# Kernel optimization log

Measured on AMD Instinct MI355X. Metric: run time of the kernel, lower is better.

Reference implementation:

```python
import jax, jax.numpy as jnp
import numpy as np

BLOCK_DIMS = [(512, 512), (512, 512), (512, 512)]
OUTPUT_SIZE = 10
BATCH = 65536
BN_EPS = 1e-5


def sign_ste(x):
    # Binarize = sign() with straight-through estimator (torch code mutates .data,
    # so autograd sees identity). Forward value is exactly jnp.sign(x).
    return x + jax.lax.stop_gradient(jnp.sign(x) - x)


def setup_inputs() -> dict:
    key = jax.random.key(0)
    ks = jax.random.split(key, 2 + 6 * len(BLOCK_DIMS) + 2)
    it = iter(ks)
    x = jax.random.normal(next(it), (BATCH, BLOCK_DIMS[0][0]), dtype=jnp.float32)
    Ws, bs, gammas, betas = [], [], [], []
    for (din, dout) in BLOCK_DIMS:
        lim = 1.0 / np.sqrt(din)
        Ws.append(jax.random.uniform(next(it), (dout, din), jnp.float32, -lim, lim))
        bs.append(jax.random.uniform(next(it), (dout,), jnp.float32, -lim, lim))
        gammas.append(jnp.ones((dout,), jnp.float32))
        betas.append(jnp.zeros((dout,), jnp.float32))
        next(it); next(it)  # burn keys for determinism symmetry
    din = BLOCK_DIMS[-1][1]
    lim = 1.0 / np.sqrt(din)
    W_out = jax.random.uniform(next(it), (OUTPUT_SIZE, din), jnp.float32, -lim, lim)
    b_out = jax.random.uniform(next(it), (OUTPUT_SIZE,), jnp.float32, -lim, lim)
    return {"x": x, "Ws": Ws, "bs": bs, "gammas": gammas, "betas": betas,
            "W_out": W_out, "b_out": b_out}


def reference(x, Ws, bs, gammas, betas, W_out, b_out):
    # x.view(-1, input_size) then Binarize(x); BinarizeLinear re-binarizes its
    # input (sign is idempotent) and binarizes its weight, keeps float bias.
    h = sign_ste(x)
    for W, b, g, be in zip(Ws, bs, gammas, betas):
        h = jnp.einsum('bi,oi->bo', sign_ste(h), sign_ste(W)) + b
        # BatchNorm1d in training mode: biased batch statistics over the batch dim
        mu = jnp.mean(h, axis=0)
        var = jnp.var(h, axis=0)
        h = (h - mu) * jax.lax.rsqrt(var + BN_EPS) * g + be
        h = jnp.clip(h, -1.0, 1.0)  # Hardtanh
    h = jnp.einsum('bi,oi->bo', sign_ste(h), sign_ste(W_out)) + b_out
    return jax.nn.log_softmax(h, axis=-1)
```

## Files before the change

kernel.cpp:

```cpp
#include <hip/hip_runtime.h>
#include <stdint.h>

typedef unsigned long long u64;
typedef unsigned int u32;

#define BATCH   65536
#define DIN     512
#define NW      8
#define NCLS    10
#define RPB     64
#define NSL     16


__device__ u64 g_bits[2][BATCH * NW];
__device__ u64 g_mask[2][BATCH * NW];
__device__ u64 g_rowflag[2][BATCH / 64];
__device__ int g_cp0[NSL * DIN + 4];
__device__ int g_cp1[NSL * DIN];
__device__ int g_S1[DIN];
__device__ int g_fastflag[4];
__device__ u64 g_wbitsT3[3][NW * DIN];
__device__ u64 g_wmaskT3[3][NW * DIN];
__device__ u64 g_obits[NCLS * NW];
__device__ u64 g_omask[NCLS * NW];

__device__ __forceinline__ int* cpbase(int sel) { return sel ? g_cp1 : g_cp0; }
#define WZ_OFF (NSL * DIN)

__global__ __launch_bounds__(512) void k_zero()
{
    const int t = blockIdx.x * 512 + threadIdx.x;
    for (int k = t; k < NSL * DIN + 4; k += 16 * 512)
        g_cp0[k] = 0;
}

__global__ __launch_bounds__(256) void k_prep_all(
    const float* __restrict__ x,
    const float* __restrict__ W0, const float* __restrict__ W1,
    const float* __restrict__ W2,
    const float* __restrict__ g0, const float* __restrict__ b0,
    const float* __restrict__ g1, const float* __restrict__ b1,
    const float* __restrict__ g2, const float* __restrict__ b2,
    const float* __restrict__ Wout)
{
    __shared__ int csB[DIN];
    __shared__ u64 AZ[4];
    const int tid = threadIdx.x, lane = tid & 63, wv = tid >> 6;
    const int b = blockIdx.x;
    const int gwave = b * 4 + wv;

    if (gwave < 3 * DIN) {
        const int layer = gwave >> 9, row = gwave & (DIN - 1);
        const float* W = (layer == 0) ? W0 : (layer == 1) ? W1 : W2;
        const float4* p = (const float4*)(W + (size_t)row * DIN + lane * 8);
        float4 v0 = p[0], v1 = p[1];
        float f[8] = {v0.x, v0.y, v0.z, v0.w, v1.x, v1.y, v1.z, v1.w};
        u32 byteS = 0, byteM = 0;
#pragma unroll
        for (int j = 0; j < 8; j++) {
            u32 pos = f[j] > 0.0f;
            u32 nz  = f[j] != 0.0f;
            byteS |= pos << j;
            byteM |= nz << j;
        }
        u64 wS = 0, wM = 0;
        const int src = (lane & 7) * 8;
#pragma unroll
        for (int j = 0; j < 8; j++) {
            wS |= (u64)(__shfl((int)byteS, src + j) & 0xFF) << (8 * j);
            wM |= (u64)(__shfl((int)byteM, src + j) & 0xFF) << (8 * j);
        }
        if (lane < 8) {
            g_wbitsT3[layer][(size_t)lane * DIN + row] = wS;
            g_wmaskT3[layer][(size_t)lane * DIN + row] = wM;
        }
        u64 ok = __ballot(byteM == 0xFFu);
        if (lane == 0 && ok != ~0ull) atomicOr(&g_cp0[WZ_OFF + layer], 1);
    } else if (gwave < 3 * DIN + NCLS) {
        const int row = gwave - 3 * DIN;
        const float4* p = (const float4*)(Wout + (size_t)row * DIN + lane * 8);
        float4 v0 = p[0], v1 = p[1];
        float f[8] = {v0.x, v0.y, v0.z, v0.w, v1.x, v1.y, v1.z, v1.w};
        u32 byteS = 0, byteM = 0;
#pragma unroll
        for (int j = 0; j < 8; j++) {
            u32 pos = f[j] > 0.0f;
            u32 nz  = f[j] != 0.0f;
            byteS |= pos << j;
            byteM |= nz << j;
        }
        u64 wS = 0, wM = 0;
        const int src = (lane & 7) * 8;
#pragma unroll
        for (int j = 0; j < 8; j++) {
            wS |= (u64)(__shfl((int)byteS, src + j) & 0xFF) << (8 * j);
            wM |= (u64)(__shfl((int)byteM, src + j) & 0xFF) << (8 * j);
        }
        if (lane < 8) {
            g_obits[row * NW + lane] = wS;
            g_omask[row * NW + lane] = wM;
        }
    } else if (gwave < 3 * DIN + NCLS + 3) {
        const int layer = gwave - (3 * DIN + NCLS);
        const float* gp = (layer == 0) ? g0 : (layer == 1) ? g1 : g2;
        const float* bp = (layer == 0) ? b0 : (layer == 1) ? b1 : b2;
        bool allok = true;
#pragma unroll
        for (int j = 0; j < 8; j++) {
            float gv = gp[j * 64 + lane], bv = bp[j * 64 + lane];
            allok &= (__ballot((gv > 0.0f) && (bv == 0.0f)) == ~0ull);
        }
        if (lane == 0) g_fastflag[layer] = allok ? 1 : 0;
    }

    for (int i = tid; i < DIN; i += 256) csB[i] = 0;
    __syncthreads();
    int cs[8];
#pragma unroll
    for (int j = 0; j < 8; j++) cs[j] = 0;
    u64 zb = 0;
    const int rbase = b * 64 + wv * 16;

    auto proc = [&](int row, int rb, float4 v0, float4 v1) {
        float f[8] = {v0.x, v0.y, v0.z, v0.w, v1.x, v1.y, v1.z, v1.w};
        u32 byteS = 0, byteM = 0;
#pragma unroll
        for (int j = 0; j < 8; j++) {
            u32 pos = f[j] > 0.0f;
            u32 nz  = f[j] != 0.0f;
            byteS |= pos << j;
            byteM |= nz << j;
            cs[j] += nz ? (pos ? 1 : -1) : 0;
        }
        u64 wS = 0, wM = 0;
        const int src = (lane & 7) * 8;
#pragma unroll
        for (int j = 0; j < 8; j++) {
            wS |= (u64)(__shfl((int)byteS, src + j) & 0xFF) << (8 * j);
            wM |= (u64)(__shfl((int)byteM, src + j) & 0xFF) << (8 * j);
        }
        u64 ok = __ballot(byteM == 0xFFu);
        if (lane < 8)
            g_bits[0][(size_t)row * NW + lane] = wS;
        if (ok != ~0ull) {
            if (lane < 8) g_mask[0][(size_t)row * NW + lane] = wM;
            zb |= 1ull << rb;
        }
    };

    for (int k = 0; k < 16; k += 2) {
        const int rowA = rbase + k, rowB = rowA + 1;
        const float4* pA = (const float4*)(x + (size_t)rowA * DIN + lane * 8);
        const float4* pB = (const float4*)(x + (size_t)rowB * DIN + lane * 8);
        float4 a0 = pA[0], a1 = pA[1];
        float4 c0 = pB[0], c1 = pB[1];
        proc(rowA, wv * 16 + k,     a0, a1);
        proc(rowB, wv * 16 + k + 1, c0, c1);
    }
#pragma unroll
    for (int j = 0; j < 8; j++)
        if (cs[j]) atomicAdd(&csB[lane * 8 + j], cs[j]);
    if (lane == 0) AZ[wv] = zb;
    __syncthreads();
    if (tid == 0) g_rowflag[0][b] = AZ[0] | AZ[1] | AZ[2] | AZ[3];
    for (int i = tid; i < DIN; i += 256) {
        int v = csB[i];
        if (v) atomicAdd(&g_cp0[(b & (NSL - 1)) * DIN + i], v);
    }
}

__global__ __launch_bounds__(512) void k_s1(int sel, int layer)
{
    const int so = sel ^ 1;
    __shared__ int csL[DIN];
    const int tid = threadIdx.x;
    const int t1 = blockIdx.x * 512 + tid;
    {
        int* cpn = cpbase(so);
        if (t1 < NSL * DIN) cpn[t1] = 0;
        if (t1 < BATCH / 64) g_rowflag[so][t1] = 0;
    }
    {
        const int* cps = cpbase(sel);
        int s = 0;
#pragma unroll
        for (int p = 0; p < NSL; p++) s += cps[p * DIN + tid];
        csL[tid] = s;
    }
    __syncthreads();
    const int lane = tid & 63, wv = tid >> 6;
    const int row = blockIdx.x * 8 + wv;
    u64 wS_h = 0, wM_h = 0;
    if (lane < 8) {
        wS_h = g_wbitsT3[layer][(size_t)lane * DIN + row];
        wM_h = g_wmaskT3[layer][(size_t)lane * DIN + row];
    }
    const u64 wS = __shfl(wS_h, lane >> 3);
    const u64 wM = __shfl(wM_h, lane >> 3);
    const u32 s8 = (u32)(wS >> (8 * (lane & 7))) & 0xFF;
    const u32 m8 = (u32)(wM >> (8 * (lane & 7))) & 0xFF;
    int acc = 0;
#pragma unroll
    for (int k = 0; k < 8; k++) {
        int c = csL[lane * 8 + k];
        int v = ((s8 >> k) & 1) ? c : -c;
        acc += ((m8 >> k) & 1) ? v : 0;
    }
#pragma unroll
    for (int o = 32; o; o >>= 1) acc += __shfl_down(acc, o);
    if (lane == 0) g_S1[row] = acc;
}

template<int FINAL>
__global__ __launch_bounds__(256, 4) void k_bingemm(int sel, int layer,
        const float* __restrict__ gamma, const float* __restrict__ beta,
        const float* __restrict__ bout, float* __restrict__ out)
{
    const int so = sel ^ 1;
    __shared__ alignas(16) u64 AT[RPB * NW];
    __shared__ u64 AZ[FINAL ? 1 : 4];
    __shared__ u64 SB[FINAL ? RPB * 9 : 1];
    __shared__ u64 SM[FINAL ? RPB * 9 : 1];
    __shared__ float ZR[FINAL ? RPB * 11 : 1];
    const int tid  = threadIdx.x;
    const int lane = tid & 63;
    const int wv   = tid >> 6;
    const int rowBase = blockIdx.x * RPB;
    const u64* wbT = g_wbitsT3[layer];
    const u64* wmT = g_wmaskT3[layer];
    int* cpo = cpbase(so);

    {
        ulonglong2* dst = (ulonglong2*)AT;
        const ulonglong2* src = (const ulonglong2*)&g_bits[sel][(size_t)rowBase * NW];
        dst[tid] = src[tid];
    }
    const int col0 = wv * 128 + lane;
    const int col1 = col0 + 64;
    u64 w0[8], w1[8];
#pragma unroll
    for (int c = 0; c < 8; c++) {
        w0[c] = wbT[c * DIN + col0];
        w1[c] = wbT[c * DIN + col1];
    }
    const int thr0 = g_S1[col0];
    const int thr1 = g_S1[col1];
    const int R0 = (DIN << 16) - thr0, R1 = (DIN << 16) - thr1;
    const int tg0 = (R0 + ((1 << 17) - 1)) >> 17, tl0 = (R0 >> 17) + 1;
    const int tg1 = (R1 + ((1 << 17) - 1)) >> 17, tl1 = (R1 >> 17) + 1;
    const u64 rflags = g_rowflag[sel][blockIdx.x];
    const bool slowAll = (g_fastflag[layer] == 0) || (g_cp0[WZ_OFF + layer] != 0);
    const bool noTie = __all((tg0 == tl0) && (tg1 == tl1));
    int cs0 = 0, cs1 = 0;
    u64 mB0 = 0, mB1 = 0, mM0 = 0, mM1 = 0;
    u64 anyz = 0;
    __syncthreads();

    if (!slowAll && rflags == 0 && noTie) {
        mM0 = ~0ull; mM1 = ~0ull;
        int n0 = 0, n1 = 0;
#pragma unroll 4
        for (int r = 0; r < RPB; r++) {
            const ulonglong2* Av = (const ulonglong2*)(AT + r * NW);
            ulonglong2 A0 = Av[0], A1 = Av[1], A2 = Av[2], A3 = Av[3];
            const u64 aw[8] = {A0.x, A0.y, A1.x, A1.y, A2.x, A2.y, A3.x, A3.y};
            int P0 = 0, P1 = 0;
#pragma unroll
            for (int c = 0; c < 8; c++) {
                P0 += __popcll(aw[c] ^ w0[c]);
                P1 += __popcll(aw[c] ^ w1[c]);
            }
            bool gb0 = P0 < tg0, gb1 = P1 < tg1;
            u64 gt0 = __ballot(gb0);
            u64 gt1 = __ballot(gb1);
            n0 += (int)gb0; n1 += (int)gb1;
            bool mine = (lane == r);
            mB0 = mine ? gt0 : mB0;  mB1 = mine ? gt1 : mB1;
        }
        cs0 = 2 * n0 - RPB;
        cs1 = 2 * n1 - RPB;
    } else if (!slowAll && rflags == 0) {
#pragma unroll 4
        for (int r = 0; r < RPB; r++) {
            const ulonglong2* Av = (const ulonglong2*)(AT + r * NW);
            ulonglong2 A0 = Av[0], A1 = Av[1], A2 = Av[2], A3 = Av[3];
            const u64 aw[8] = {A0.x, A0.y, A1.x, A1.y, A2.x, A2.y, A3.x, A3.y};
            int P0 = 0, P1 = 0;
#pragma unroll
            for (int c = 0; c < 8; c++) {
                P0 += __popcll(aw[c] ^ w0[c]);
                P1 += __popcll(aw[c] ^ w1[c]);
            }
            bool gb0 = P0 < tg0, lb0 = P0 >= tl0;
            bool gb1 = P1 < tg1, lb1 = P1 >= tl1;
            u64 gt0 = __ballot(gb0), nz0 = gt0 | __ballot(lb0);
            u64 gt1 = __ballot(gb1), nz1 = gt1 | __ballot(lb1);
            cs0 += (int)gb0 - (int)lb0;
            cs1 += (int)gb1 - (int)lb1;
            bool mine = (lane == r);
            mB0 = mine ? gt0 : mB0;  mB1 = mine ? gt1 : mB1;
            mM0 = mine ? nz0 : mM0;  mM1 = mine ? nz1 : mM1;
            if ((nz0 & nz1) != ~0ull) {
                anyz |= 1ull << r;
                if (lane == 0)
                    atomicOr(&g_rowflag[so][(rowBase + r) >> 6],
                             1ull << ((rowBase + r) & 63));
            }
        }
    } else {
        double td0 = 0.0, td1 = 0.0;
        int md0 = 0, md1 = 0;
        {
            float g = gamma[col0], be = beta[col0];
            int S1v = thr0;
            td0 = (double)S1v;
            if (g != 0.0f) {
                md0 = (g > 0.0f) ? 0 : 1;
                if (be != 0.0f) {
                    double s = rsqrt((double)DIN + 1e-5);
                    td0 = (double)S1v - 65536.0 * (double)be / (s * (double)g);
                }
            } else md0 = (be > 0.0f) ? 2 : ((be < 0.0f) ? 3 : 4);
            g = gamma[col1]; be = beta[col1]; S1v = thr1;
            td1 = (double)S1v;
            if (g != 0.0f) {
                md1 = (g > 0.0f) ? 0 : 1;
                if (be != 0.0f) {
                    double s = rsqrt((double)DIN + 1e-5);
                    td1 = (double)S1v - 65536.0 * (double)be / (s * (double)g);
                }
            } else md1 = (be > 0.0f) ? 2 : ((be < 0.0f) ? 3 : 4);
        }
        for (int r = 0; r < RPB; r++) {
            const bool fl = (rflags >> r) & 1;
            int bit0, bit1;
            if (!slowAll && !fl) {
                int P0 = 0, P1 = 0;
#pragma unroll
                for (int c = 0; c < 8; c++) {
                    u64 a = AT[r * NW + c];
                    P0 += __popcll(a ^ w0[c]);
                    P1 += __popcll(a ^ w1[c]);
                }
                int v0 = (DIN - 2 * P0) << 16;
                int v1 = (DIN - 2 * P1) << 16;
                bit0 = (v0 > thr0) - (v0 < thr0);
                bit1 = (v1 > thr1) - (v1 < thr1);
            } else {
                const int row = rowBase + r;
                int P0 = 0, Q0 = 0, P1 = 0, Q1 = 0;
#pragma unroll
                for (int c = 0; c < 8; c++) {
                    u64 a  = AT[r * NW + c];
                    u64 am = fl ? g_mask[sel][(size_t)row * NW + c] : ~0ull;
                    u64 m0 = am & wmT[c * DIN + col0];
                    u64 m1 = am & wmT[c * DIN + col1];
                    P0 += __popcll((a ^ w0[c]) & m0);  Q0 += __popcll(m0);
                    P1 += __popcll((a ^ w1[c]) & m1);  Q1 += __popcll(m1);
                }
                double Ds0 = (double)(Q0 - 2 * P0) * 65536.0;
                double Ds1 = (double)(Q1 - 2 * P1) * 65536.0;
                int c0 = (Ds0 > td0) ? 1 : ((Ds0 < td0) ? -1 : 0);
                int c1 = (Ds1 > td1) ? 1 : ((Ds1 < td1) ? -1 : 0);
                bit0 = (md0 == 0) ? c0 : (md0 == 1) ? -c0
                     : (md0 == 2) ? 1 : (md0 == 3) ? -1 : 0;
                bit1 = (md1 == 0) ? c1 : (md1 == 1) ? -c1
                     : (md1 == 2) ? 1 : (md1 == 3) ? -1 : 0;
            }
            u64 gt0 = __ballot(bit0 > 0), nz0 = __ballot(bit0 != 0);
            u64 gt1 = __ballot(bit1 > 0), nz1 = __ballot(bit1 != 0);
            cs0 += bit0;
            cs1 += bit1;
            bool mine = (lane == r);
            mB0 = mine ? gt0 : mB0;  mB1 = mine ? gt1 : mB1;
            mM0 = mine ? nz0 : mM0;  mM1 = mine ? nz1 : mM1;
            if ((nz0 & nz1) != ~0ull) {
                anyz |= 1ull << r;
                if (lane == 0)
                    atomicOr(&g_rowflag[so][(rowBase + r) >> 6],
                             1ull << ((rowBase + r) & 63));
            }
        }
    }

    if constexpr (FINAL) {
        SB[lane * 9 + 2 * wv]     = mB0;
        SB[lane * 9 + 2 * wv + 1] = mB1;
        SM[lane * 9 + 2 * wv]     = mM0;
        SM[lane * 9 + 2 * wv + 1] = mM1;
        __syncthreads();
        u64 b[NW], m[NW];
#pragma unroll
        for (int c = 0; c < NW; c++) { b[c] = SB[lane * 9 + c]; m[c] = SM[lane * 9 + c]; }
        const int cls0 = (wv < 2) ? wv * 3 : 2 + wv * 2;
        const int ncl  = (wv < 2) ? 3 : 2;
        for (int k = 0; k < ncl; k++) {
            const int o = cls0 + k;
            int P = 0, P2 = 0;
#pragma unroll
            for (int c = 0; c < NW; c++) {
                u64 om = g_omask[o * NW + c];
                u64 mm = m[c] & om;
                P  += __popcll((b[c] ^ g_obits[o * NW + c]) & mm);
                P2 += __popcll(mm);
            }
            ZR[lane * 11 + o] = (float)(P2 - 2 * P) + bout[o];
        }
        __syncthreads();
        if (wv == 0) {
            float z[NCLS], mx = -1e30f;
#pragma unroll
            for (int o = 0; o < NCLS; o++) { z[o] = ZR[lane * 11 + o]; mx = fmaxf(mx, z[o]); }
            float s = 0.0f;
#pragma unroll
            for (int o = 0; o < NCLS; o++) s += expf(z[o] - mx);
            float l = logf(s);
            float2* o2 = (float2*)(out + (size_t)(rowBase + lane) * NCLS);
#pragma unroll
            for (int p = 0; p < 5; p++) {
                float2 v;
                v.x = z[2 * p]     - mx - l;
                v.y = z[2 * p + 1] - mx - l;
                o2[p] = v;
            }
        }
    } else {
        AZ[wv] = anyz;
        __syncthreads();
        const u64 rowz = AZ[0] | AZ[1] | AZ[2] | AZ[3];
        size_t bofs = (size_t)(rowBase + lane) * NW + 2 * wv;
        ulonglong2 vb; vb.x = mB0; vb.y = mB1;
        *(ulonglong2*)&g_bits[so][bofs] = vb;
        if ((rowz >> lane) & 1) {
            ulonglong2 vm; vm.x = mM0; vm.y = mM1;
            *(ulonglong2*)&g_mask[so][bofs] = vm;
        }
        atomicAdd(&cpo[(blockIdx.x & (NSL - 1)) * DIN + col0], cs0);
        atomicAdd(&cpo[(blockIdx.x & (NSL - 1)) * DIN + col1], cs1);
    }
}

extern "C" void kernel_launch(void* const* d_in, const int* in_sizes, int n_in,
                              void* d_out, int out_size, void* d_ws, size_t ws_size,
                              hipStream_t stream)
{
    const float *x = 0, *Wl[3] = {0,0,0}, *gl[3] = {0,0,0}, *bl[3] = {0,0,0};
    const float *Wout = 0, *bout = 0;
    {
        int i = 0;
        x = (const float*)d_in[i++];
        if (i < n_in && in_sizes[i] == 3 * DIN * DIN) {
            for (int l = 0; l < 3; l++) Wl[l] = (const float*)d_in[i] + (size_t)l * DIN * DIN;
            i++;
        } else {
            for (int l = 0; l < 3 && i < n_in; l++) Wl[l] = (const float*)d_in[i++];
        }
        if (i < n_in && in_sizes[i] == 3 * DIN) i++;
        else i += 3;
        if (i < n_in && in_sizes[i] == 3 * DIN) {
            for (int l = 0; l < 3; l++) gl[l] = (const float*)d_in[i] + (size_t)l * DIN;
            i++;
        } else {
            for (int l = 0; l < 3 && i < n_in; l++) gl[l] = (const float*)d_in[i++];
        }
        if (i < n_in && in_sizes[i] == 3 * DIN) {
            for (int l = 0; l < 3; l++) bl[l] = (const float*)d_in[i] + (size_t)l * DIN;
            i++;
        } else {
            for (int l = 0; l < 3 && i < n_in; l++) bl[l] = (const float*)d_in[i++];
        }
        if (i < n_in) Wout = (const float*)d_in[i++];
        if (i < n_in) bout = (const float*)d_in[i++];
    }
    float* out = (float*)d_out;
    (void)out_size; (void)d_ws; (void)ws_size;

    k_zero<<<16, 512, 0, stream>>>();
    k_prep_all<<<1024, 256, 0, stream>>>(x, Wl[0], Wl[1], Wl[2],
                                         gl[0], bl[0], gl[1], bl[1], gl[2], bl[2],
                                         Wout);
    k_s1<<<64, 512, 0, stream>>>(0, 0);
    k_bingemm<0><<<BATCH / RPB, 256, 0, stream>>>(0, 0, gl[0], bl[0], bout, out);
    k_s1<<<64, 512, 0, stream>>>(1, 1);
    k_bingemm<0><<<BATCH / RPB, 256, 0, stream>>>(1, 1, gl[1], bl[1], bout, out);
    k_s1<<<64, 512, 0, stream>>>(0, 2);
    k_bingemm<1><<<BATCH / RPB, 256, 0, stream>>>(0, 2, gl[2], bl[2], bout, out);
}
```

Before: 338.9 us.

## Fold column-sum reduction into last-finishing block of preceding kernels

Removes the separate zeroing kernel and the three small k_s1 launches. The last block to finish each of prep and the first two GEMM layers, found through an atomic counter, now does the column-sum reduction and threshold computation. Zeroing of the counters and partial sums moves to the tail of the final GEMM, so the next call starts from clean state. The x-loading loop also issues four rows of loads per iteration instead of two. This cuts launch gaps, but one block now runs a serial tail of 512 rows on 256 threads, and correctness relies on the state left by the previous invocation.

```diff
diff --git a/kernel.cpp b/kernel.cpp
--- a/kernel.cpp
+++ b/kernel.cpp
@@ -15,8 +15,9 @@
 __device__ u64 g_bits[2][BATCH * NW];
 __device__ u64 g_mask[2][BATCH * NW];
 __device__ u64 g_rowflag[2][BATCH / 64];
-__device__ int g_cp0[NSL * DIN + 4];
+__device__ int g_cp0[NSL * DIN + 16];
 __device__ int g_cp1[NSL * DIN];
+__device__ int g_wzstash;
 __device__ int g_S1[DIN];
 __device__ int g_fastflag[4];
 __device__ u64 g_wbitsT3[3][NW * DIN];
@@ -25,13 +26,48 @@
 __device__ u64 g_omask[NCLS * NW];
 
 __device__ __forceinline__ int* cpbase(int sel) { return sel ? g_cp1 : g_cp0; }
-#define WZ_OFF (NSL * DIN)
-
-__global__ __launch_bounds__(512) void k_zero()
+#define WZ_OFF   (NSL * DIN)
+#define CNT_PREP (WZ_OFF + 4)
+#define CNT_G0   (WZ_OFF + 5)
+#define CNT_G1   (WZ_OFF + 6)
+#define CP0_TOT  (NSL * DIN + 16)
+
+__device__ void s1_tail(const int* __restrict__ cps, int layer,
+                        int* __restrict__ cpn, u64* __restrict__ rfn)
 {
-    const int t = blockIdx.x * 512 + threadIdx.x;
-    for (int k = t; k < NSL * DIN + 4; k += 16 * 512)
-        g_cp0[k] = 0;
+    __shared__ int csL[DIN];
+    const int tid = threadIdx.x;
+    for (int k = tid; k < NSL * DIN; k += 256) cpn[k] = 0;
+    for (int k = tid; k < BATCH / 64; k += 256) rfn[k] = 0;
+    for (int i = tid; i < DIN; i += 256) {
+        int s = 0;
+#pragma unroll
+        for (int p = 0; p < NSL; p++) s += cps[p * DIN + i];
+        csL[i] = s;
+    }
+    __syncthreads();
+    const int lane = tid & 63, wv = tid >> 6;
+    for (int row = wv; row < DIN; row += 4) {
+        u64 wS_h = 0, wM_h = 0;
+        if (lane < 8) {
+            wS_h = g_wbitsT3[layer][(size_t)lane * DIN + row];
+            wM_h = g_wmaskT3[layer][(size_t)lane * DIN + row];
+        }
+        const u64 wS = __shfl(wS_h, lane >> 3);
+        const u64 wM = __shfl(wM_h, lane >> 3);
+        const u32 s8 = (u32)(wS >> (8 * (lane & 7))) & 0xFF;
+        const u32 m8 = (u32)(wM >> (8 * (lane & 7))) & 0xFF;
+        int acc = 0;
+#pragma unroll
+        for (int k = 0; k < 8; k++) {
+            int c = csL[lane * 8 + k];
+            int v = ((s8 >> k) & 1) ? c : -c;
+            acc += ((m8 >> k) & 1) ? v : 0;
+        }
+#pragma unroll
+        for (int o = 32; o; o >>= 1) acc += __shfl_down(acc, o);
+        if (lane == 0) g_S1[row] = acc;
+    }
 }
 
 __global__ __launch_bounds__(256) void k_prep_all(
@@ -45,6 +81,7 @@
 {
     __shared__ int csB[DIN];
     __shared__ u64 AZ[4];
+    __shared__ int s_last;
     const int tid = threadIdx.x, lane = tid & 63, wv = tid >> 6;
     const int b = blockIdx.x;
     const int gwave = b * 4 + wv;
@@ -148,14 +185,20 @@
         }
     };
 
-    for (int k = 0; k < 16; k += 2) {
-        const int rowA = rbase + k, rowB = rowA + 1;
-        const float4* pA = (const float4*)(x + (size_t)rowA * DIN + lane * 8);
-        const float4* pB = (const float4*)(x + (size_t)rowB * DIN + lane * 8);
-        float4 a0 = pA[0], a1 = pA[1];
-        float4 c0 = pB[0], c1 = pB[1];
-        proc(rowA, wv * 16 + k,     a0, a1);
-        proc(rowB, wv * 16 + k + 1, c0, c1);
+    for (int k = 0; k < 16; k += 4) {
+        const int r0 = rbase + k;
+        const float4* p0 = (const float4*)(x + (size_t)r0 * DIN + lane * 8);
+        const float4* p1 = (const float4*)(x + (size_t)(r0 + 1) * DIN + lane * 8);
+        const float4* p2 = (const float4*)(x + (size_t)(r0 + 2) * DIN + lane * 8);
+        const float4* p3 = (const float4*)(x + (size_t)(r0 + 3) * DIN + lane * 8);
+        float4 a0 = p0[0], a1 = p0[1];
+        float4 b0v = p1[0], b1v = p1[1];
+        float4 c0 = p2[0], c1 = p2[1];
+        float4 d0 = p3[0], d1 = p3[1];
+        proc(r0,     wv * 16 + k,     a0, a1);
+        proc(r0 + 1, wv * 16 + k + 1, b0v, b1v);
+        proc(r0 + 2, wv * 16 + k + 2, c0, c1);
+        proc(r0 + 3, wv * 16 + k + 3, d0, d1);
     }
 #pragma unroll
     for (int j = 0; j < 8; j++)
@@ -167,48 +210,15 @@
         int v = csB[i];
         if (v) atomicAdd(&g_cp0[(b & (NSL - 1)) * DIN + i], v);
     }
-}
-
-__global__ __launch_bounds__(512) void k_s1(int sel, int layer)
-{
-    const int so = sel ^ 1;
-    __shared__ int csL[DIN];
-    const int tid = threadIdx.x;
-    const int t1 = blockIdx.x * 512 + tid;
-    {
-        int* cpn = cpbase(so);
-        if (t1 < NSL * DIN) cpn[t1] = 0;
-        if (t1 < BATCH / 64) g_rowflag[so][t1] = 0;
-    }
-    {
-        const int* cps = cpbase(sel);
-        int s = 0;
-#pragma unroll
-        for (int p = 0; p < NSL; p++) s += cps[p * DIN + tid];
-        csL[tid] = s;
-    }
+
+    __threadfence();
+    if (tid == 0)
+        s_last = (atomicAdd(&g_cp0[CNT_PREP], 1) == (int)gridDim.x - 1) ? 1 : 0;
     __syncthreads();
-    const int lane = tid & 63, wv = tid >> 6;
-    const int row = blockIdx.x * 8 + wv;
-    u64 wS_h = 0, wM_h = 0;
-    if (lane < 8) {
-        wS_h = g_wbitsT3[layer][(size_t)lane * DIN + row];
-        wM_h = g_wmaskT3[layer][(size_t)lane * DIN + row];
-    }
-    const u64 wS = __shfl(wS_h, lane >> 3);
-    const u64 wM = __shfl(wM_h, lane >> 3);
-    const u32 s8 = (u32)(wS >> (8 * (lane & 7))) & 0xFF;
-    const u32 m8 = (u32)(wM >> (8 * (lane & 7))) & 0xFF;
-    int acc = 0;
-#pragma unroll
-    for (int k = 0; k < 8; k++) {
-        int c = csL[lane * 8 + k];
-        int v = ((s8 >> k) & 1) ? c : -c;
-        acc += ((m8 >> k) & 1) ? v : 0;
-    }
-#pragma unroll
-    for (int o = 32; o; o >>= 1) acc += __shfl_down(acc, o);
-    if (lane == 0) g_S1[row] = acc;
+    if (s_last) {
+        __threadfence();
+        s1_tail(g_cp0, 0, g_cp1, g_rowflag[1]);
+    }
 }
 
 template<int FINAL>
@@ -222,6 +232,7 @@
     __shared__ u64 SB[FINAL ? RPB * 9 : 1];
     __shared__ u64 SM[FINAL ? RPB * 9 : 1];
     __shared__ float ZR[FINAL ? RPB * 11 : 1];
+    __shared__ int s_last;
     const int tid  = threadIdx.x;
     const int lane = tid & 63;
     const int wv   = tid >> 6;
@@ -249,7 +260,8 @@
     const int tg0 = (R0 + ((1 << 17) - 1)) >> 17, tl0 = (R0 >> 17) + 1;
     const int tg1 = (R1 + ((1 << 17) - 1)) >> 17, tl1 = (R1 >> 17) + 1;
     const u64 rflags = g_rowflag[sel][blockIdx.x];
-    const bool slowAll = (g_fastflag[layer] == 0) || (g_cp0[WZ_OFF + layer] != 0);
+    const int wzv = FINAL ? g_wzstash : g_cp0[WZ_OFF + layer];
+    const bool slowAll = (g_fastflag[layer] == 0) || (wzv != 0);
     const bool noTie = __all((tg0 == tl0) && (tg1 == tl1));
     int cs0 = 0, cs1 = 0;
     u64 mB0 = 0, mB1 = 0, mM0 = 0, mM1 = 0;
@@ -424,6 +436,11 @@
                 o2[p] = v;
             }
         }
+        if (blockIdx.x < 17) {
+            const int base = blockIdx.x * 512;
+            for (int k = base + tid; k < CP0_TOT && k < base + 512; k += 256)
+                g_cp0[k] = 0;
+        }
     } else {
         AZ[wv] = anyz;
         __syncthreads();
@@ -437,6 +454,17 @@
         }
         atomicAdd(&cpo[(blockIdx.x & (NSL - 1)) * DIN + col0], cs0);
         atomicAdd(&cpo[(blockIdx.x & (NSL - 1)) * DIN + col1], cs1);
+
+        __threadfence();
+        if (tid == 0)
+            s_last = (atomicAdd(&g_cp0[(layer == 0) ? CNT_G0 : CNT_G1], 1)
+                      == (int)gridDim.x - 1) ? 1 : 0;
+        __syncthreads();
+        if (s_last) {
+            __threadfence();
+            if (layer == 1 && tid == 0) g_wzstash = g_cp0[WZ_OFF + 2];
+            s1_tail(cpbase(so), layer + 1, cpbase(sel), g_rowflag[sel]);
+        }
     }
 }
 
@@ -475,14 +503,10 @@
     float* out = (float*)d_out;
     (void)out_size; (void)d_ws; (void)ws_size;
 
-    k_zero<<<16, 512, 0, stream>>>();
     k_prep_all<<<1024, 256, 0, stream>>>(x, Wl[0], Wl[1], Wl[2],
                                          gl[0], bl[0], gl[1], bl[1], gl[2], bl[2],
                                          Wout);
-    k_s1<<<64, 512, 0, stream>>>(0, 0);
     k_bingemm<0><<<BATCH / RPB, 256, 0, stream>>>(0, 0, gl[0], bl[0], bout, out);
-    k_s1<<<64, 512, 0, stream>>>(1, 1);
     k_bingemm<0><<<BATCH / RPB, 256, 0, stream>>>(1, 1, gl[1], bl[1], bout, out);
-    k_s1<<<64, 512, 0, stream>>>(0, 2);
     k_bingemm<1><<<BATCH / RPB, 256, 0, stream>>>(0, 2, gl[2], bl[2], bout, out);
 }
```

Measured after the change: 838.6 us. +147.5%, slower.
